# Performance work log

Measured on AMD Instinct MI355X. Metric: run time of the kernel, lower is better.

The kernel has to match this reference:

```python
import jax, jax.numpy as jnp
import numpy as np

B, S, HID, NH = 2, 2048, 2048, 16
HD = HID // NH  # 128


def setup_inputs() -> dict:
    key = jax.random.key(0)
    ks = jax.random.split(key, 6)
    xav = lambda k, shape: jax.random.uniform(k, shape, jnp.float32,
        -jnp.sqrt(6.0 / (shape[0] + shape[1])), jnp.sqrt(6.0 / (shape[0] + shape[1])))
    return {
        'hidden_state': jax.random.normal(ks[0], (B, S, HID), jnp.float32),
        'attention_mask': jnp.ones((B, 1, 1, S), jnp.int32),
        'Wq': xav(ks[1], (HID, HID)), 'bq': jnp.zeros((HID,), jnp.float32),
        'Wk': xav(ks[2], (HD, HID)),  'bk': jnp.zeros((HD,), jnp.float32),
        'Wv': xav(ks[3], (HD, HID)),  'bv': jnp.zeros((HD,), jnp.float32),
        'Wo': xav(ks[4], (HID, HID)), 'bo': jnp.zeros((HID,), jnp.float32),
    }


def reference(hidden_state, attention_mask, Wq, bq, Wk, bk, Wv, bv, Wo, bo):
    b, s, _ = hidden_state.shape
    scale = 1.0 / jnp.sqrt(jnp.float32(HD))
    # projections (torch Linear: y = x @ W.T + b)
    q = hidden_state @ Wq.T + bq                      # (B,S,HID)
    k = hidden_state @ Wk.T + bk                      # (B,S,HD) single KV head
    v = hidden_state @ Wv.T + bv                      # (B,S,HD)
    q = q.reshape(b, s, NH, HD).transpose(0, 2, 1, 3)  # (B,H,S,D)
    # scores with shared KV head broadcast over query heads
    scores = jnp.einsum('bhqd,bkd->bhqk', q, k) * scale  # (B,H,S,S)
    scores = jnp.where(attention_mask == 0, -jnp.inf, scores)
    probs = jax.nn.softmax(scores, axis=-1)
    out = jnp.einsum('bhqk,bkd->bhqd', probs, v)       # (B,H,S,D)
    out = out.transpose(0, 2, 1, 3).reshape(b, s, HID)
    return out @ Wo.T + bo
```

## Files before the change

### kernel.cpp

```cpp
#include <hip/hip_runtime.h>

#define B_   2
#define S_   2048
#define HID_ 2048
#define NH_  16
#define HD_  128
#define M_   (B_ * S_)

using half4   = __attribute__((ext_vector_type(4))) _Float16;
using half8   = __attribute__((ext_vector_type(8))) _Float16;
using floatx4 = __attribute__((ext_vector_type(4))) float;

__device__ __forceinline__ void gl_lds16(const void* g, void* l) {
  __builtin_amdgcn_global_load_lds(
      (const __attribute__((address_space(1))) void*)g,
      (__attribute__((address_space(3))) void*)l, 16, 0, 0);
}

__device__ __forceinline__ void cvt8(const float* s, _Float16* d, int i) {
  const floatx4* sp = (const floatx4*)s;
  floatx4 a = sp[(size_t)i * 2];
  floatx4 b = sp[(size_t)i * 2 + 1];
  half8 h;
  h[0] = (_Float16)a[0]; h[1] = (_Float16)a[1];
  h[2] = (_Float16)a[2]; h[3] = (_Float16)a[3];
  h[4] = (_Float16)b[0]; h[5] = (_Float16)b[1];
  h[6] = (_Float16)b[2]; h[7] = (_Float16)b[3];
  *(half8*)(d + (size_t)i * 8) = h;
}

__global__ __launch_bounds__(256) void cvt_all(
    const float* __restrict__ h,  const float* __restrict__ wq,
    const float* __restrict__ wk, const float* __restrict__ wv,
    const float* __restrict__ wo,
    _Float16* __restrict__ dh,  _Float16* __restrict__ dwq,
    _Float16* __restrict__ dwk, _Float16* __restrict__ dwv,
    _Float16* __restrict__ dwo) {
  int bid = blockIdx.x;
  const float* s;
  _Float16* d;
  int off;
  if (bid < 4096)      { s = h;  d = dh;  off = bid; }
  else if (bid < 6144) { s = wq; d = dwq; off = bid - 4096; }
  else if (bid < 6272) { s = wk; d = dwk; off = bid - 6144; }
  else if (bid < 6400) { s = wv; d = dwv; off = bid - 6272; }
  else                 { s = wo; d = dwo; off = bid - 6400; }
  cvt8(s, d, off * 256 + threadIdx.x);
}

template <typename OutT, bool TRANS>
__device__ __forceinline__ void gemm128_body(
    const _Float16* __restrict__ A, const _Float16* __restrict__ W,
    const float* __restrict__ bias, OutT* __restrict__ C,
    int Nout, int K, int m0, int n0w, int c0) {
  __shared__ __align__(16) _Float16 As[128][32];
  __shared__ __align__(16) _Float16 Ws[128][32];

  const int tid  = threadIdx.x;
  const int lane = tid & 63;
  const int wave = tid >> 6;
  const int wm   = wave >> 1, wn = wave & 1;
  const int l15  = lane & 15, lq = lane >> 4;
  const int srow = wave * 16 + (lane >> 2);
  const int scol = (lane & 3) * 8;

  floatx4 acc[4][4];
#pragma unroll
  for (int i = 0; i < 4; i++)
#pragma unroll
    for (int j = 0; j < 4; j++) acc[i][j] = (floatx4){0.f, 0.f, 0.f, 0.f};

  const _Float16* Ag = A + (size_t)(m0 + srow) * K + scol;
  const _Float16* Wg = W + (size_t)(n0w + srow) * K + scol;
  const size_t step64 = (size_t)64 * K;

  for (int kt = 0; kt < K; kt += 32) {
    gl_lds16(Ag + kt,          &As[wave * 16][0]);
    gl_lds16(Ag + step64 + kt, &As[64 + wave * 16][0]);
    gl_lds16(Wg + kt,          &Ws[wave * 16][0]);
    gl_lds16(Wg + step64 + kt, &Ws[64 + wave * 16][0]);
    __syncthreads();

    half8 af[4], bf[4];
#pragma unroll
    for (int i = 0; i < 4; i++)
      af[i] = *(const half8*)&As[wm * 64 + i * 16 + l15][lq * 8];
#pragma unroll
    for (int j = 0; j < 4; j++)
      bf[j] = *(const half8*)&Ws[wn * 64 + j * 16 + l15][lq * 8];
#pragma unroll
    for (int i = 0; i < 4; i++)
#pragma unroll
      for (int j = 0; j < 4; j++)
        acc[i][j] = __builtin_amdgcn_mfma_f32_16x16x32_f16(af[i], bf[j], acc[i][j], 0, 0, 0);
    __syncthreads();
  }

  const int rq = lq * 4;
  if constexpr (TRANS) {
    const int b  = m0 / S_;
    const int sb = m0 - b * S_ + wm * 64;
#pragma unroll
    for (int j = 0; j < 4; j++) {
      int col  = wn * 64 + j * 16 + l15;
      float bv = bias[n0w + col];
#pragma unroll
      for (int i = 0; i < 4; i++) {
        half4 o;
#pragma unroll
        for (int r = 0; r < 4; r++) o[r] = (_Float16)(acc[i][j][r] + bv);
        *(half4*)((_Float16*)C + (size_t)b * HD_ * S_ + (size_t)col * S_
                  + sb + i * 16 + rq) = o;
      }
    }
  } else {
#pragma unroll
    for (int j = 0; j < 4; j++) {
      int col_l = wn * 64 + j * 16 + l15;
      float bv  = bias[n0w + col_l];
#pragma unroll
      for (int i = 0; i < 4; i++) {
        int row = m0 + wm * 64 + i * 16 + rq;
#pragma unroll
        for (int r = 0; r < 4; r++)
          C[(size_t)(row + r) * Nout + c0 + col_l] = (OutT)(acc[i][j][r] + bv);
      }
    }
  }
}

__global__ __launch_bounds__(256) void gemm_qkv(
    const _Float16* __restrict__ A,
    const _Float16* __restrict__ Wq, const float* __restrict__ bq, _Float16* __restrict__ Qh,
    const _Float16* __restrict__ Wk, const float* __restrict__ bk, _Float16* __restrict__ Kh,
    const _Float16* __restrict__ Wv, const float* __restrict__ bv, _Float16* __restrict__ VhT) {
  const int nt = blockIdx.x, m0 = blockIdx.y * 128;
  if (nt < 16)
    gemm128_body<_Float16, false>(A, Wq, bq, Qh, HID_, HID_, m0, nt * 128, nt * 128);
  else if (nt == 16)
    gemm128_body<_Float16, false>(A, Wk, bk, Kh, HD_, HID_, m0, 0, 0);
  else
    gemm128_body<_Float16, true>(A, Wv, bv, VhT, HD_, HID_, m0, 0, 0);
}

__global__ __launch_bounds__(256) void gemm_out(
    const _Float16* __restrict__ A, const _Float16* __restrict__ W,
    const float* __restrict__ bias, float* __restrict__ C) {
  gemm128_body<float, false>(A, W, bias, C, HID_, HID_, blockIdx.y * 128,
                             blockIdx.x * 128, blockIdx.x * 128);
}

__global__ __launch_bounds__(256, 2) void attn_mfma(
    const _Float16* __restrict__ Q, const _Float16* __restrict__ K,
    const _Float16* __restrict__ VhT, const int* __restrict__ mask,
    _Float16* __restrict__ Obuf) {
  constexpr int BN = 64, KP = 136, VP = 72, NT = S_ / BN;
  __shared__ __align__(16) _Float16 Ks[2][BN][KP];
  __shared__ __align__(16) _Float16 Vt[2][HD_][VP];

  const int tid  = threadIdx.x;
  const int lane = tid & 63, wave = tid >> 6;
  const int l15  = lane & 15, lq = lane >> 4;
  const int q0   = blockIdx.x * 128;
  const int b    = blockIdx.y >> 4, h = blockIdx.y & 15;
  const float sl2e = 0.08838834764831845f * 1.44269504088896341f;
  const _Float16* VT = VhT + (size_t)b * HD_ * S_;
  const _Float16* Kb = K + (size_t)b * S_ * HD_;
  const int* mb = mask + b * S_;

  int krow[4], kcol[4], vrow[4], vcol[4];
#pragma unroll
  for (int it = 0; it < 4; it++) {
    int i = it * 256 + tid;
    krow[it] = i >> 4;       kcol[it] = (i & 15) * 8;
    vrow[it] = i >> 3;       vcol[it] = (i & 7) * 8;
  }

  half8 qf[2][4];
#pragma unroll
  for (int i = 0; i < 2; i++)
#pragma unroll
    for (int kd = 0; kd < 4; kd++)
      qf[i][kd] = *(const half8*)(Q + (size_t)(b * S_ + q0 + wave * 32 + i * 16 + l15) * HID_
                                  + h * HD_ + kd * 32 + lq * 8);

  float m_i[2] = {-3.0e38f, -3.0e38f};
  float l_i[2] = {0.f, 0.f};
  floatx4 oacc[2][8];
#pragma unroll
  for (int i = 0; i < 2; i++)
#pragma unroll
    for (int jd = 0; jd < 8; jd++) oacc[i][jd] = (floatx4){0.f, 0.f, 0.f, 0.f};

  half8 kreg[4], vreg[4];
#pragma unroll
  for (int it = 0; it < 4; it++) {
    kreg[it] = *(const half8*)(Kb + (size_t)krow[it] * HD_ + kcol[it]);
    vreg[it] = *(const half8*)(VT + (size_t)vrow[it] * S_ + vcol[it]);
  }
#pragma unroll
  for (int it = 0; it < 4; it++) {
    *(half8*)&Ks[0][krow[it]][kcol[it]] = kreg[it];
    *(half8*)&Vt[0][vrow[it]][vcol[it]] = vreg[it];
  }
  __syncthreads();

  for (int t = 0; t < NT; t++) {
    const int cur = t & 1;
    const int n0  = t * BN;
    const bool has_next = (t + 1) < NT;

    if (has_next) {
      const int nn = n0 + BN;
#pragma unroll
      for (int it = 0; it < 4; it++) {
        kreg[it] = *(const half8*)(Kb + (size_t)(nn + krow[it]) * HD_ + kcol[it]);
        vreg[it] = *(const half8*)(VT + (size_t)vrow[it] * S_ + nn + vcol[it]);
      }
    }

    int4 mk4[4];
#pragma unroll
    for (int j = 0; j < 4; j++)
      mk4[j] = *(const int4*)(mb + n0 + j * 16 + lq * 4);

    floatx4 st[4][2];
#pragma unroll
    for (int j = 0; j < 4; j++)
#pragma unroll
      for (int i = 0; i < 2; i++) st[j][i] = (floatx4){0.f, 0.f, 0.f, 0.f};
#pragma unroll
    for (int kd = 0; kd < 4; kd++) {
      half8 kb[4];
#pragma unroll
      for (int j = 0; j < 4; j++)
        kb[j] = *(const half8*)&Ks[cur][j * 16 + l15][kd * 32 + lq * 8];
#pragma unroll
      for (int j = 0; j < 4; j++)
#pragma unroll
        for (int i = 0; i < 2; i++)
          st[j][i] = __builtin_amdgcn_mfma_f32_16x16x32_f16(kb[j], qf[i][kd], st[j][i], 0, 0, 0);
    }

    floatx4 amf[4];
#pragma unroll
    for (int j = 0; j < 4; j++) {
      amf[j][0] = mk4[j].x ? 0.f : -3.0e38f;
      amf[j][1] = mk4[j].y ? 0.f : -3.0e38f;
      amf[j][2] = mk4[j].z ? 0.f : -3.0e38f;
      amf[j][3] = mk4[j].w ? 0.f : -3.0e38f;
    }

    half4 ph[2][4];
#pragma unroll
    for (int i = 0; i < 2; i++) {
      float mx = -3.0e38f;
#pragma unroll
      for (int j = 0; j < 4; j++)
#pragma unroll
        for (int r = 0; r < 4; r++) {
          float v = st[j][i][r] * sl2e + amf[j][r];
          st[j][i][r] = v;
          mx = fmaxf(mx, v);
        }
      mx = fmaxf(mx, __shfl_xor(mx, 16));
      mx = fmaxf(mx, __shfl_xor(mx, 32));
      float mnew  = fmaxf(m_i[i], mx);
      float alpha = __builtin_amdgcn_exp2f(m_i[i] - mnew);
      m_i[i] = mnew;
      float rs = 0.f;
#pragma unroll
      for (int j = 0; j < 4; j++)
#pragma unroll
        for (int r = 0; r < 4; r++) {
          float pv = __builtin_amdgcn_exp2f(st[j][i][r] - mnew);
          ph[i][j][r] = (_Float16)pv;
          rs += pv;
        }
      rs += __shfl_xor(rs, 16);
      rs += __shfl_xor(rs, 32);
      l_i[i] = l_i[i] * alpha + rs;
#pragma unroll
      for (int r = 0; r < 4; r++) {
        float a_r = __shfl(alpha, lq * 4 + r);
#pragma unroll
        for (int jd = 0; jd < 8; jd++) oacc[i][jd][r] *= a_r;
      }
    }

#pragma unroll
    for (int j = 0; j < 4; j++) {
#pragma unroll
      for (int jd = 0; jd < 8; jd++) {
        half4 vb = *(const half4*)&Vt[cur][jd * 16 + l15][j * 16 + lq * 4];
#pragma unroll
        for (int i = 0; i < 2; i++)
          oacc[i][jd] = __builtin_amdgcn_mfma_f32_16x16x16f16(ph[i][j], vb, oacc[i][jd], 0, 0, 0);
      }
    }

    if (has_next) {
      const int nxt = 1 - cur;
#pragma unroll
      for (int it = 0; it < 4; it++) {
        *(half8*)&Ks[nxt][krow[it]][kcol[it]] = kreg[it];
        *(half8*)&Vt[nxt][vrow[it]][vcol[it]] = vreg[it];
      }
    }
    __syncthreads();
  }

#pragma unroll
  for (int i = 0; i < 2; i++) {
    float linv = 1.0f / l_i[i];
#pragma unroll
    for (int r = 0; r < 4; r++) {
      float lr = __shfl(linv, lq * 4 + r);
      size_t row = (size_t)(b * S_ + q0 + wave * 32 + i * 16 + lq * 4 + r);
#pragma unroll
      for (int jd = 0; jd < 8; jd++)
        Obuf[row * HID_ + h * HD_ + jd * 16 + l15] = (_Float16)(oacc[i][jd][r] * lr);
    }
  }
}

extern "C" void kernel_launch(void* const* d_in, const int* in_sizes, int n_in,
                              void* d_out, int out_size, void* d_ws, size_t ws_size,
                              hipStream_t stream) {
  const float* hidden = (const float*)d_in[0];
  const int*   mask   = (const int*)d_in[1];
  const float* Wq = (const float*)d_in[2];
  const float* bq = (const float*)d_in[3];
  const float* Wk = (const float*)d_in[4];
  const float* bk = (const float*)d_in[5];
  const float* Wv = (const float*)d_in[6];
  const float* bv = (const float*)d_in[7];
  const float* Wo = (const float*)d_in[8];
  const float* bo = (const float*)d_in[9];
  float* out = (float*)d_out;

  char* p = (char*)d_ws;
  auto alloc = [&](size_t bytes) {
    char* r = p;
    p += (bytes + 255) & ~(size_t)255;
    return r;
  };
  _Float16* hidh = (_Float16*)alloc((size_t)M_ * HID_ * 2);
  _Float16* Wqh  = (_Float16*)alloc((size_t)HID_ * HID_ * 2);
  _Float16* Wkh  = (_Float16*)alloc((size_t)HD_ * HID_ * 2);
  _Float16* Wvh  = (_Float16*)alloc((size_t)HD_ * HID_ * 2);
  _Float16* Woh  = (_Float16*)alloc((size_t)HID_ * HID_ * 2);
  _Float16* Qh   = (_Float16*)alloc((size_t)M_ * HID_ * 2);
  _Float16* Kh   = (_Float16*)alloc((size_t)M_ * HD_ * 2);
  _Float16* VhT  = (_Float16*)alloc((size_t)M_ * HD_ * 2);
  _Float16* attnh = (_Float16*)alloc((size_t)M_ * HID_ * 2);

  cvt_all<<<8448, 256, 0, stream>>>(hidden, Wq, Wk, Wv, Wo,
                                    hidh, Wqh, Wkh, Wvh, Woh);

  dim3 gqkv(18, M_ / 128);
  gemm_qkv<<<gqkv, 256, 0, stream>>>(hidh, Wqh, bq, Qh, Wkh, bk, Kh, Wvh, bv, VhT);

  dim3 ga(S_ / 128, B_ * NH_);
  attn_mfma<<<ga, 256, 0, stream>>>(Qh, Kh, VhT, mask, attnh);

  dim3 go(HID_ / 128, M_ / 128);
  gemm_out<<<go, 256, 0, stream>>>(attnh, Woh, bo, out);
}
```

Before: 327.1 us.

## Split attention over key halves with separate combine kernel

Splits the attention kernel along the key dimension into two halves. Each half writes an unnormalized fp16 partial output plus per-row max and sum statistics, and a new combine kernel merges the halves into the attention buffer. The aim is to double the block count and occupancy (launch bounds raised to 4), with LDS single-buffered to fit. In exchange it adds a large partial-output write and read, an extra kernel launch, and an extra barrier per tile in place of double buffering.

```diff
diff --git a/kernel.cpp b/kernel.cpp
--- a/kernel.cpp
+++ b/kernel.cpp
@@ -150,19 +150,20 @@
                              blockIdx.x * 128, blockIdx.x * 128);
 }
 
-__global__ __launch_bounds__(256, 2) void attn_mfma(
+__global__ __launch_bounds__(256, 4) void attn_split(
     const _Float16* __restrict__ Q, const _Float16* __restrict__ K,
     const _Float16* __restrict__ VhT, const int* __restrict__ mask,
-    _Float16* __restrict__ Obuf) {
-  constexpr int BN = 64, KP = 136, VP = 72, NT = S_ / BN;
-  __shared__ __align__(16) _Float16 Ks[2][BN][KP];
-  __shared__ __align__(16) _Float16 Vt[2][HD_][VP];
+    _Float16* __restrict__ Po, float2* __restrict__ stats) {
+  constexpr int BN = 64, KP = 136, VP = 72, HT = (S_ / BN) / 2;
+  __shared__ __align__(16) _Float16 Ks[BN][KP];
+  __shared__ __align__(16) _Float16 Vt[HD_][VP];
 
   const int tid  = threadIdx.x;
   const int lane = tid & 63, wave = tid >> 6;
   const int l15  = lane & 15, lq = lane >> 4;
   const int q0   = blockIdx.x * 128;
   const int b    = blockIdx.y >> 4, h = blockIdx.y & 15;
+  const int z    = blockIdx.z;
   const float sl2e = 0.08838834764831845f * 1.44269504088896341f;
   const _Float16* VT = VhT + (size_t)b * HD_ * S_;
   const _Float16* Kb = K + (size_t)b * S_ * HD_;
@@ -172,8 +173,8 @@
 #pragma unroll
   for (int it = 0; it < 4; it++) {
     int i = it * 256 + tid;
-    krow[it] = i >> 4;       kcol[it] = (i & 15) * 8;
-    vrow[it] = i >> 3;       vcol[it] = (i & 7) * 8;
+    krow[it] = i >> 4;  kcol[it] = (i & 15) * 8;
+    vrow[it] = i >> 3;  vcol[it] = (i & 7) * 8;
   }
 
   half8 qf[2][4];
@@ -185,30 +186,30 @@
                                   + h * HD_ + kd * 32 + lq * 8);
 
   float m_i[2] = {-3.0e38f, -3.0e38f};
-  float l_i[2] = {0.f, 0.f};
+  float l_p[2] = {0.f, 0.f};
   floatx4 oacc[2][8];
 #pragma unroll
   for (int i = 0; i < 2; i++)
 #pragma unroll
     for (int jd = 0; jd < 8; jd++) oacc[i][jd] = (floatx4){0.f, 0.f, 0.f, 0.f};
 
+  const int n_base = z * HT * BN;
   half8 kreg[4], vreg[4];
 #pragma unroll
   for (int it = 0; it < 4; it++) {
-    kreg[it] = *(const half8*)(Kb + (size_t)krow[it] * HD_ + kcol[it]);
-    vreg[it] = *(const half8*)(VT + (size_t)vrow[it] * S_ + vcol[it]);
+    kreg[it] = *(const half8*)(Kb + (size_t)(n_base + krow[it]) * HD_ + kcol[it]);
+    vreg[it] = *(const half8*)(VT + (size_t)vrow[it] * S_ + n_base + vcol[it]);
   }
 #pragma unroll
   for (int it = 0; it < 4; it++) {
-    *(half8*)&Ks[0][krow[it]][kcol[it]] = kreg[it];
-    *(half8*)&Vt[0][vrow[it]][vcol[it]] = vreg[it];
+    *(half8*)&Ks[krow[it]][kcol[it]] = kreg[it];
+    *(half8*)&Vt[vrow[it]][vcol[it]] = vreg[it];
   }
   __syncthreads();
 
-  for (int t = 0; t < NT; t++) {
-    const int cur = t & 1;
-    const int n0  = t * BN;
-    const bool has_next = (t + 1) < NT;
+  for (int t = 0; t < HT; t++) {
+    const int n0 = n_base + t * BN;
+    const bool has_next = (t + 1) < HT;
 
     if (has_next) {
       const int nn = n0 + BN;
@@ -234,7 +235,7 @@
       half8 kb[4];
 #pragma unroll
       for (int j = 0; j < 4; j++)
-        kb[j] = *(const half8*)&Ks[cur][j * 16 + l15][kd * 32 + lq * 8];
+        kb[j] = *(const half8*)&Ks[j * 16 + l15][kd * 32 + lq * 8];
 #pragma unroll
       for (int j = 0; j < 4; j++)
 #pragma unroll
@@ -277,9 +278,7 @@
           ph[i][j][r] = (_Float16)pv;
           rs += pv;
         }
-      rs += __shfl_xor(rs, 16);
-      rs += __shfl_xor(rs, 32);
-      l_i[i] = l_i[i] * alpha + rs;
+      l_p[i] = l_p[i] * alpha + rs;
 #pragma unroll
       for (int r = 0; r < 4; r++) {
         float a_r = __shfl(alpha, lq * 4 + r);
@@ -292,7 +291,7 @@
     for (int j = 0; j < 4; j++) {
 #pragma unroll
       for (int jd = 0; jd < 8; jd++) {
-        half4 vb = *(const half4*)&Vt[cur][jd * 16 + l15][j * 16 + lq * 4];
+        half4 vb = *(const half4*)&Vt[jd * 16 + l15][j * 16 + lq * 4];
 #pragma unroll
         for (int i = 0; i < 2; i++)
           oacc[i][jd] = __builtin_amdgcn_mfma_f32_16x16x16f16(ph[i][j], vb, oacc[i][jd], 0, 0, 0);
@@ -300,28 +299,68 @@
     }
 
     if (has_next) {
-      const int nxt = 1 - cur;
+      __syncthreads();
 #pragma unroll
       for (int it = 0; it < 4; it++) {
-        *(half8*)&Ks[nxt][krow[it]][kcol[it]] = kreg[it];
-        *(half8*)&Vt[nxt][vrow[it]][vcol[it]] = vreg[it];
-      }
-    }
-    __syncthreads();
-  }
-
+        *(half8*)&Ks[krow[it]][kcol[it]] = kreg[it];
+        *(half8*)&Vt[vrow[it]][vcol[it]] = vreg[it];
+      }
+      __syncthreads();
+    }
+  }
+
+  float l_f[2];
 #pragma unroll
   for (int i = 0; i < 2; i++) {
-    float linv = 1.0f / l_i[i];
+    float l = l_p[i];
+    l += __shfl_xor(l, 16);
+    l += __shfl_xor(l, 32);
+    l_f[i] = l;
+  }
+  _Float16* Ob = Po + (size_t)z * M_ * HID_;
+#pragma unroll
+  for (int i = 0; i < 2; i++) {
 #pragma unroll
     for (int r = 0; r < 4; r++) {
-      float lr = __shfl(linv, lq * 4 + r);
       size_t row = (size_t)(b * S_ + q0 + wave * 32 + i * 16 + lq * 4 + r);
 #pragma unroll
       for (int jd = 0; jd < 8; jd++)
-        Obuf[row * HID_ + h * HD_ + jd * 16 + l15] = (_Float16)(oacc[i][jd][r] * lr);
-    }
-  }
+        Ob[row * HID_ + h * HD_ + jd * 16 + l15] = (_Float16)oacc[i][jd][r];
+    }
+  }
+  if (lq == 0) {
+#pragma unroll
+    for (int i = 0; i < 2; i++) {
+      int s = q0 + wave * 32 + i * 16 + l15;
+      stats[((size_t)(z * B_ + b) * NH_ + h) * S_ + s] = make_float2(m_i[i], l_f[i]);
+    }
+  }
+}
+
+__global__ __launch_bounds__(256) void attn_combine(
+    const _Float16* __restrict__ Po, const float2* __restrict__ stats,
+    _Float16* __restrict__ attnh) {
+  int gi  = blockIdx.x * 256 + threadIdx.x;
+  int row = gi >> 8;
+  int c8  = (gi & 255) * 8;
+  int b   = row >> 11;
+  int s   = row & (S_ - 1);
+  int hh  = c8 >> 7;
+  float2 s1 = stats[((size_t)(0 * B_ + b) * NH_ + hh) * S_ + s];
+  float2 s2 = stats[((size_t)(1 * B_ + b) * NH_ + hh) * S_ + s];
+  float M  = fmaxf(s1.x, s2.x);
+  float w1 = __builtin_amdgcn_exp2f(s1.x - M);
+  float w2 = __builtin_amdgcn_exp2f(s2.x - M);
+  float inv = 1.0f / (w1 * s1.y + w2 * s2.y);
+  w1 *= inv; w2 *= inv;
+  size_t off = (size_t)row * HID_ + c8;
+  half8 a = *(const half8*)(Po + off);
+  half8 c = *(const half8*)(Po + (size_t)M_ * HID_ + off);
+  half8 o;
+#pragma unroll
+  for (int j = 0; j < 8; j++)
+    o[j] = (_Float16)(w1 * (float)a[j] + w2 * (float)c[j]);
+  *(half8*)(attnh + off) = o;
 }
 
 extern "C" void kernel_launch(void* const* d_in, const int* in_sizes, int n_in,
@@ -345,15 +384,17 @@
     p += (bytes + 255) & ~(size_t)255;
     return r;
   };
-  _Float16* hidh = (_Float16*)alloc((size_t)M_ * HID_ * 2);
-  _Float16* Wqh  = (_Float16*)alloc((size_t)HID_ * HID_ * 2);
-  _Float16* Wkh  = (_Float16*)alloc((size_t)HD_ * HID_ * 2);
-  _Float16* Wvh  = (_Float16*)alloc((size_t)HD_ * HID_ * 2);
-  _Float16* Woh  = (_Float16*)alloc((size_t)HID_ * HID_ * 2);
-  _Float16* Qh   = (_Float16*)alloc((size_t)M_ * HID_ * 2);
-  _Float16* Kh   = (_Float16*)alloc((size_t)M_ * HD_ * 2);
-  _Float16* VhT  = (_Float16*)alloc((size_t)M_ * HD_ * 2);
+  _Float16* hidh  = (_Float16*)alloc((size_t)M_ * HID_ * 2);
+  _Float16* Wqh   = (_Float16*)alloc((size_t)HID_ * HID_ * 2);
+  _Float16* Wkh   = (_Float16*)alloc((size_t)HD_ * HID_ * 2);
+  _Float16* Wvh   = (_Float16*)alloc((size_t)HD_ * HID_ * 2);
+  _Float16* Woh   = (_Float16*)alloc((size_t)HID_ * HID_ * 2);
+  _Float16* Qh    = (_Float16*)alloc((size_t)M_ * HID_ * 2);
+  _Float16* Kh    = (_Float16*)alloc((size_t)M_ * HD_ * 2);
+  _Float16* VhT   = (_Float16*)alloc((size_t)M_ * HD_ * 2);
   _Float16* attnh = (_Float16*)alloc((size_t)M_ * HID_ * 2);
+  _Float16* Po    = (_Float16*)alloc((size_t)2 * M_ * HID_ * 2);
+  float2*   stats = (float2*)alloc((size_t)2 * B_ * NH_ * S_ * sizeof(float2));
 
   cvt_all<<<8448, 256, 0, stream>>>(hidden, Wq, Wk, Wv, Wo,
                                     hidh, Wqh, Wkh, Wvh, Woh);
@@ -361,8 +402,9 @@
   dim3 gqkv(18, M_ / 128);
   gemm_qkv<<<gqkv, 256, 0, stream>>>(hidh, Wqh, bq, Qh, Wkh, bk, Kh, Wvh, bv, VhT);
 
-  dim3 ga(S_ / 128, B_ * NH_);
-  attn_mfma<<<ga, 256, 0, stream>>>(Qh, Kh, VhT, mask, attnh);
+  dim3 ga(S_ / 128, B_ * NH_, 2);
+  attn_split<<<ga, 256, 0, stream>>>(Qh, Kh, VhT, mask, Po, stats);
+  attn_combine<<<(M_ * HID_ / 8 + 255) / 256, 256, 0, stream>>>(Po, stats, attnh);
 
   dim3 go(HID_ / 128, M_ / 128);
   gemm_out<<<go, 256, 0, stream>>>(attnh, Woh, bo, out);
```

Result: slower. 715.7 us (+118.8%).
